# Optimization experiments

Measured on AMD Instinct MI355X. Metric: run time of the kernel, lower is better.

The kernel has to match this reference:

```python
import jax, jax.numpy as jnp
import numpy as np

N, E, F, EF, D, G = 25000, 100000, 32, 8, 64, 1000


def setup_inputs() -> dict:
    key = jax.random.key(0)
    ks = jax.random.split(key, 32)
    p = lambda k, shape: (jax.random.normal(k, shape, jnp.float32) * 0.05)
    inp = {
        "x": jax.random.normal(ks[0], (N, F), jnp.float32),
        "edge_index": jax.random.randint(ks[1], (2, E), 0, N, jnp.int64 if jax.config.jax_enable_x64 else jnp.int32),
        "edge_attr": jax.random.uniform(ks[2], (E, EF), jnp.float32),
        "batch": jnp.sort(jax.random.randint(ks[3], (N,), 0, G, jnp.int32)),
        # lin0
        "W0": p(ks[4], (F, D)), "b0": p(ks[5], (D,)),
        # edge MLP: Linear(EF, D) -> ReLU -> Linear(D, D*D)
        "We1": p(ks[6], (EF, D)), "be1": p(ks[7], (D,)),
        "We2": p(ks[8], (D, D * D)), "be2": p(ks[9], (D * D,)),
        # NNConv root weight + bias
        "Wroot": p(ks[10], (D, D)), "bconv": p(ks[11], (D,)),
        # GRU (single layer): gate order r, z, n
        "Wi": p(ks[12], (3 * D, D)), "Wh": p(ks[13], (3 * D, D)),
        "bi": p(ks[14], (3 * D,)), "bh": p(ks[15], (3 * D,)),
        # heads
        "W11": p(ks[16], (D, D)), "b11": p(ks[17], (D,)),
        "W12": p(ks[18], (D, D)), "b12": p(ks[19], (D,)),
        "W13": p(ks[20], (D, 1)), "b13": p(ks[21], (1,)),
        "W21": p(ks[22], (D, D)), "b21": p(ks[23], (D,)),
        "W22": p(ks[24], (D, D)), "b22": p(ks[25], (D,)),
        "W23": p(ks[26], (D, 1)), "b23": p(ks[27], (1,)),
    }
    return inp


def reference(x, edge_index, edge_attr, batch,
              W0, b0, We1, be1, We2, be2, Wroot, bconv,
              Wi, Wh, bi, bh,
              W11, b11, W12, b12, W13, b13,
              W21, b21, W22, b22, W23, b23):
    src, dst = edge_index[0], edge_index[1]
    # lin0 + relu
    x1 = jax.nn.relu(x @ W0 + b0)                      # [N, D]
    h = x1                                              # GRU hidden init
    # NNConv: dynamic per-edge weight via edge MLP
    ew = (jax.nn.relu(edge_attr @ We1 + be1) @ We2 + be2).reshape(E, D, D)
    msg = jnp.einsum('ei,eio->eo', x1[src], ew)        # per-edge matmul
    agg = jax.ops.segment_sum(msg, dst, num_segments=N)
    x2 = jax.nn.relu(x1 @ Wroot + agg + bconv)         # [N, D]
    # GRU single step (torch gate order: r, z, n)
    gi = x2 @ Wi.T + bi
    gh = h @ Wh.T + bh
    r = jax.nn.sigmoid(gi[:, :D] + gh[:, :D])
    z = jax.nn.sigmoid(gi[:, D:2 * D] + gh[:, D:2 * D])
    n = jnp.tanh(gi[:, 2 * D:] + r * gh[:, 2 * D:])
    hn = (1.0 - z) * n + z * h                          # [N, D]
    # graph pooling (scatter_add over batch)
    pooled = jax.ops.segment_sum(hn, batch, num_segments=G)  # [G, D]
    # two MLP heads
    x_1 = jax.nn.relu(pooled @ W11 + b11)
    x_1 = jax.nn.relu(x_1 @ W12 + b12)
    x_1 = x_1 @ W13 + b13
    x_2 = jax.nn.relu(pooled @ W21 + b21)
    x_2 = jax.nn.relu(x_2 @ W22 + b22)
    x_2 = x_2 @ W23 + b23
    return jnp.concatenate([x_1, x_2], axis=1)          # [G, 2]
```

## Files before the change

kernel.cpp:

```cpp
#include <hip/hip_runtime.h>
#include <hip/hip_bf16.h>
#include <hip/hip_fp16.h>

#define NN 25000
#define NE 100000
#define FIN 32
#define DD 64
#define NG 1000

typedef unsigned short u16;
typedef __attribute__((ext_vector_type(8))) short short8;
typedef __attribute__((ext_vector_type(8))) _Float16 f16x8;
typedef __attribute__((ext_vector_type(4))) float f32x4;

__device__ __forceinline__ u16 f2h(float f) {
    __half h = __float2half(f);
    return __builtin_bit_cast(u16, h);
}
__device__ __forceinline__ float h2f(u16 u) {
    __half h = __builtin_bit_cast(__half, u);
    return __half2float(h);
}
__device__ __forceinline__ f16x8 s2h(short8 v) { return __builtin_bit_cast(f16x8, v); }
__device__ __forceinline__ bool idx_is_i64(const int* e) {
    return (e[1] == 0) & (e[3] == 0) & (e[5] == 0) & (e[7] == 0) & (e[9] == 0);
}
__device__ __forceinline__ int ld_src(const int* e, int i, bool i64) {
    return i64 ? e[2 * i] : e[i];
}
__device__ __forceinline__ int ld_dst(const int* e, int i, bool i64) {
    return i64 ? e[2 * (NE + i)] : e[NE + i];
}

__global__ __launch_bounds__(256) void k_pre(const float* __restrict__ x,
                                             const float* __restrict__ W0,
                                             const float* __restrict__ b0,
                                             u16* __restrict__ x1b,
                                             const float* __restrict__ We2,
                                             const float* __restrict__ be2,
                                             float* __restrict__ agg,
                                             float* __restrict__ pooled,
                                             u16* __restrict__ Bt2,
                                             const float* __restrict__ Wi,
                                             const float* __restrict__ Wh,
                                             const float* __restrict__ Wroot,
                                             u16* __restrict__ Wib,
                                             u16* __restrict__ Whb,
                                             u16* __restrict__ Wrb,
                                             const float* __restrict__ W11,
                                             const float* __restrict__ W12,
                                             const float* __restrict__ W21,
                                             const float* __restrict__ W22,
                                             u16* __restrict__ W11b,
                                             u16* __restrict__ W12b,
                                             u16* __restrict__ W21b,
                                             u16* __restrict__ W22b) {
    __shared__ float sbuf[4096 + 512];
    int tid = threadIdx.x;
    if (blockIdx.x < 1563) {
        float* sW = sbuf;
        float* sx = sbuf + 4096;
        for (int i = tid; i < FIN * DD; i += 256) sW[i] = W0[i];
        int nbase = blockIdx.x * 16;
        for (int i = tid; i < 16 * FIN; i += 256) {
            int nl = i >> 5, f = i & 31;
            int n = nbase + nl;
            sx[i] = (n < NN) ? x[n * FIN + f] : 0.f;
        }
        __syncthreads();
        int lane = tid & 63, nl = tid >> 6;
        float bias = b0[lane];
        #pragma unroll
        for (int rr = 0; rr < 4; rr++) {
            int row = nl * 4 + rr;
            int n = nbase + row;
            if (n < NN) {
                float acc = bias;
                #pragma unroll
                for (int f = 0; f < FIN; f++) acc += sx[row * FIN + f] * sW[f * DD + lane];
                x1b[n * DD + lane] = f2h(fmaxf(acc, 0.f));
            }
        }
    } else if (blockIdx.x < 1628) {
        int kc = blockIdx.x - 1563;
        const float* src = (kc < 64) ? (We2 + kc * 4096) : be2;
        for (int i = tid; i < 4096; i += 256) sbuf[i] = src[i];
        __syncthreads();
        for (int m = tid; m < 4096; m += 256) {
            int f = m >> 9, ln = (m >> 3) & 63, j = m & 7;
            int s = f >> 2, c = f & 3;
            int o = c * 16 + (ln & 15);
            int rlow = s * 32 + (ln >> 4) * 8 + j;
            Bt2[kc * 4096 + m] = f2h(sbuf[rlow * 64 + o]);
        }
    } else {
        int tid0 = (blockIdx.x - 1628) * 256 + threadIdx.x;
        const int STR = 256 * 256;
        for (int i = tid0; i < NN * DD; i += STR) agg[i] = 0.f;
        for (int i = tid0; i < NG * DD; i += STR) pooled[i] = 0.f;
        for (int i = tid0; i < 12288; i += STR) {
            int fr = i >> 9, lane = (i >> 3) & 63, j = i & 7;
            int c = fr >> 1, kcx = fr & 1;
            int row = c * 16 + (lane & 15);
            int col = kcx * 32 + (lane >> 4) * 8 + j;
            Wib[i] = f2h(Wi[row * 64 + col]);
            Whb[i] = f2h(Wh[row * 64 + col]);
        }
        for (int i = tid0; i < 4096; i += STR) {
            int fr = i >> 9, lane = (i >> 3) & 63, j = i & 7;
            int c = fr >> 1, kcx = fr & 1;
            int row = c * 16 + (lane & 15);
            int col = kcx * 32 + (lane >> 4) * 8 + j;
            int idx = col * 64 + row;
            Wrb[i]  = f2h(Wroot[idx]);
            W11b[i] = f2h(W11[idx]);
            W12b[i] = f2h(W12[idx]);
            W21b[i] = f2h(W21[idx]);
            W22b[i] = f2h(W22[idx]);
        }
    }
}

__global__ __launch_bounds__(512, 4) void k_msg(const float* __restrict__ ea,
                                                const int* __restrict__ eidx,
                                                const float* __restrict__ We1,
                                                const float* __restrict__ be1,
                                                const u16* __restrict__ x1b,
                                                const u16* __restrict__ Bt2,
                                                float* __restrict__ agg) {
    __shared__ __align__(16) u16 sX[128 * 72];
    __shared__ __align__(16) u16 sTh[65 * 128 + 64];
    __shared__ float sWe1[8 * 64];
    __shared__ float sbe1[64];
    __shared__ int sDst[128];
    const int tid = threadIdx.x;
    const int lane = tid & 63, wv = tid >> 6;
    const int ll = lane & 15, quad = lane >> 4;
    const int rh = wv >> 2, cq = wv & 3;
    const int e0 = blockIdx.x * 128;
    const bool i64 = idx_is_i64(eidx);

    if (tid < 512) sWe1[tid] = We1[tid];
    if (tid < 64) sbe1[tid] = be1[tid];
    if (tid < 128) {
        sDst[tid] = (e0 + tid < NE) ? ld_dst(eidx, e0 + tid, i64) : 0;
        sTh[64 * 128 + tid] = 0x3C00;
    }

    const int el4 = tid >> 2, seg = tid & 3;
    const int eg4 = e0 + el4;
    {
        if (eg4 < NE) {
            int sv = ld_src(eidx, eg4, i64);
            const u16* xr = x1b + sv * 64 + seg * 16;
            *(uint4*)&sX[el4 * 72 + seg * 16]     = *(const uint4*)(xr);
            *(uint4*)&sX[el4 * 72 + seg * 16 + 8] = *(const uint4*)(xr + 8);
        } else {
            uint4 z = make_uint4(0, 0, 0, 0);
            *(uint4*)&sX[el4 * 72 + seg * 16]     = z;
            *(uint4*)&sX[el4 * 72 + seg * 16 + 8] = z;
        }
    }
    float eav[8];
    if (eg4 < NE) {
        f32x4 v0 = *(const f32x4*)(ea + eg4 * 8);
        f32x4 v1 = *(const f32x4*)(ea + eg4 * 8 + 4);
        #pragma unroll
        for (int f = 0; f < 4; f++) { eav[f] = v0[f]; eav[4 + f] = v1[f]; }
    } else {
        #pragma unroll
        for (int f = 0; f < 8; f++) eav[f] = 0.f;
    }
    __syncthreads();

    {
        int k0 = seg * 16;
        for (int kk = 0; kk < 16; kk++) {
            int k = k0 + kk;
            float acc = sbe1[k];
            #pragma unroll
            for (int f = 0; f < 8; f++) acc += eav[f] * sWe1[f * 64 + k];
            sTh[k * 128 + el4] = f2h((eg4 < NE) ? fmaxf(acc, 0.f) : 0.f);
        }
    }
    __syncthreads();

    short8 xa[4][2];
    #pragma unroll
    for (int rt = 0; rt < 4; rt++)
        #pragma unroll
        for (int s = 0; s < 2; s++)
            xa[rt][s] = *(const short8*)&sX[(rh * 64 + rt * 16 + ll) * 72 + s * 32 + quad * 8];

    f32x4 msg[4];
    #pragma unroll
    for (int rt = 0; rt < 4; rt++) msg[rt] = (f32x4){0.f, 0.f, 0.f, 0.f};

    const u16* gB0 = Bt2 + (0 * 4 + cq) * 512 + lane * 8;
    const u16* gB1 = Bt2 + (1 * 4 + cq) * 512 + lane * 8;
    const f32x4 zero = (f32x4){0.f, 0.f, 0.f, 0.f};
    const int tkoff = rh * 64 + quad * 4;

    #define LDR(dst, kcv, rtv) dst = *(const uint2*)&sTh[(kcv) * 128 + tkoff + (rtv) * 16];
    #define CVT(t, raw)                                                      \
        {                                                                    \
            __half2 _a = __builtin_bit_cast(__half2, (raw).x);               \
            __half2 _b = __builtin_bit_cast(__half2, (raw).y);               \
            float2 _fa = __half22float2(_a);                                 \
            float2 _fb = __half22float2(_b);                                 \
            t = (f32x4){_fa.x, _fa.y, _fb.x, _fb.y};                         \
        }

    short8 c00 = *(const short8*)(gB0);
    short8 c01 = *(const short8*)(gB1);
    short8 c10 = *(const short8*)(gB0 + 4096);
    short8 c11 = *(const short8*)(gB1 + 4096);
    uint2 tkA[4], tkB[4];
    #pragma unroll
    for (int rt = 0; rt < 4; rt++) LDR(tkA[rt], 0, rt);

    for (int kc = 0; kc < 62; kc += 2) {
        short8 n00 = *(const short8*)(gB0 + (kc + 2) * 4096);
        short8 n01 = *(const short8*)(gB1 + (kc + 2) * 4096);
        short8 n10 = *(const short8*)(gB0 + (kc + 3) * 4096);
        short8 n11 = *(const short8*)(gB1 + (kc + 3) * 4096);
        #pragma unroll
        for (int rt = 0; rt < 4; rt++) LDR(tkB[rt], kc + 1, rt);
        #pragma unroll
        for (int rt = 0; rt < 4; rt++) {
            f32x4 q0 = __builtin_amdgcn_mfma_f32_16x16x32_f16(s2h(xa[rt][0]), s2h(c00), zero, 0, 0, 0);
            f32x4 q1 = __builtin_amdgcn_mfma_f32_16x16x32_f16(s2h(xa[rt][1]), s2h(c01), zero, 0, 0, 0);
            f32x4 t; CVT(t, tkA[rt]);
            msg[rt] += t * q0;
            msg[rt] += t * q1;
        }
        #pragma unroll
        for (int rt = 0; rt < 4; rt++) LDR(tkA[rt], kc + 2, rt);
        #pragma unroll
        for (int rt = 0; rt < 4; rt++) {
            f32x4 q0 = __builtin_amdgcn_mfma_f32_16x16x32_f16(s2h(xa[rt][0]), s2h(c10), zero, 0, 0, 0);
            f32x4 q1 = __builtin_amdgcn_mfma_f32_16x16x32_f16(s2h(xa[rt][1]), s2h(c11), zero, 0, 0, 0);
            f32x4 t; CVT(t, tkB[rt]);
            msg[rt] += t * q0;
            msg[rt] += t * q1;
        }
        c00 = n00; c01 = n01; c10 = n10; c11 = n11;
    }
    {
        short8 n00 = *(const short8*)(gB0 + 64 * 4096);
        short8 n01 = *(const short8*)(gB1 + 64 * 4096);
        #pragma unroll
        for (int rt = 0; rt < 4; rt++) LDR(tkB[rt], 63, rt);
        #pragma unroll
        for (int rt = 0; rt < 4; rt++) {
            f32x4 q0 = __builtin_amdgcn_mfma_f32_16x16x32_f16(s2h(xa[rt][0]), s2h(c00), zero, 0, 0, 0);
            f32x4 q1 = __builtin_amdgcn_mfma_f32_16x16x32_f16(s2h(xa[rt][1]), s2h(c01), zero, 0, 0, 0);
            f32x4 t; CVT(t, tkA[rt]);
            msg[rt] += t * q0;
            msg[rt] += t * q1;
        }
        #pragma unroll
        for (int rt = 0; rt < 4; rt++) LDR(tkA[rt], 64, rt);
        #pragma unroll
        for (int rt = 0; rt < 4; rt++) {
            f32x4 q0 = __builtin_amdgcn_mfma_f32_16x16x32_f16(s2h(xa[rt][0]), s2h(c10), zero, 0, 0, 0);
            f32x4 q1 = __builtin_amdgcn_mfma_f32_16x16x32_f16(s2h(xa[rt][1]), s2h(c11), zero, 0, 0, 0);
            f32x4 t; CVT(t, tkB[rt]);
            msg[rt] += t * q0;
            msg[rt] += t * q1;
        }
        #pragma unroll
        for (int rt = 0; rt < 4; rt++) {
            f32x4 q0 = __builtin_amdgcn_mfma_f32_16x16x32_f16(s2h(xa[rt][0]), s2h(n00), zero, 0, 0, 0);
            f32x4 q1 = __builtin_amdgcn_mfma_f32_16x16x32_f16(s2h(xa[rt][1]), s2h(n01), zero, 0, 0, 0);
            f32x4 t; CVT(t, tkA[rt]);
            msg[rt] += t * q0;
            msg[rt] += t * q1;
        }
    }
    #undef LDR
    #undef CVT

    #pragma unroll
    for (int rt = 0; rt < 4; rt++) {
        #pragma unroll
        for (int r = 0; r < 4; r++) {
            int el = rh * 64 + rt * 16 + quad * 4 + r;
            int eg = e0 + el;
            if (eg < NE) {
                int d = sDst[el];
                atomicAdd(&agg[d * 64 + cq * 16 + ll], msg[rt][r]);
            }
        }
    }
}

__global__ __launch_bounds__(256) void k_gru(const u16* __restrict__ x1b,
                                             const float* __restrict__ agg,
                                             const u16* __restrict__ Wib,
                                             const u16* __restrict__ Whb,
                                             const u16* __restrict__ Wrb,
                                             const float* __restrict__ bconv,
                                             const float* __restrict__ bi,
                                             const float* __restrict__ bh,
                                             const int* __restrict__ batch,
                                             float* __restrict__ pooled) {
    __shared__ __align__(16) u16 sX2[64 * 72];
    __shared__ float hbuf[64 * 65];
    __shared__ int sBatch[64];
    const int tid = threadIdx.x;
    const int lane = tid & 63, wv = tid >> 6;
    const int ll = lane & 15, quad = lane >> 4;
    const int n0 = blockIdx.x * 64;

    if (tid < 64) {
        int n = n0 + tid;
        sBatch[tid] = (n < NN) ? batch[n] : -1;
    }

    short8 ha[2];
    {
        int n = n0 + wv * 16 + ll;
        #pragma unroll
        for (int kc = 0; kc < 2; kc++) {
            if (n < NN) ha[kc] = *(const short8*)(x1b + n * 64 + kc * 32 + quad * 8);
            else        ha[kc] = (short8){0,0,0,0,0,0,0,0};
        }
    }
    f32x4 acc1[4];
    #pragma unroll
    for (int c = 0; c < 4; c++) acc1[c] = (f32x4){0.f, 0.f, 0.f, 0.f};
    #pragma unroll
    for (int kc = 0; kc < 2; kc++) {
        #pragma unroll
        for (int c = 0; c < 4; c++) {
            short8 b = *(const short8*)&Wrb[(c * 2 + kc) * 512 + lane * 8];
            acc1[c] = __builtin_amdgcn_mfma_f32_16x16x32_f16(s2h(ha[kc]), s2h(b), acc1[c], 0, 0, 0);
        }
    }
    #pragma unroll
    for (int c = 0; c < 4; c++) {
        int col = c * 16 + ll;
        float bcv = bconv[col];
        #pragma unroll
        for (int r = 0; r < 4; r++) {
            int row = wv * 16 + quad * 4 + r;
            int n = n0 + row;
            float v = 0.f;
            if (n < NN) v = fmaxf(acc1[c][r] + agg[n * 64 + col] + bcv, 0.f);
            sX2[row * 72 + col] = f2h(v);
        }
    }
    __syncthreads();

    short8 xa[2];
    #pragma unroll
    for (int kc = 0; kc < 2; kc++)
        xa[kc] = *(const short8*)&sX2[(wv * 16 + ll) * 72 + kc * 32 + quad * 8];

    f32x4 agi[12], agh[12];
    #pragma unroll
    for (int c = 0; c < 12; c++) { agi[c] = (f32x4){0.f,0.f,0.f,0.f}; agh[c] = (f32x4){0.f,0.f,0.f,0.f}; }
    #pragma unroll
    for (int kc = 0; kc < 2; kc++) {
        #pragma unroll
        for (int c = 0; c < 12; c++) {
            short8 bi8 = *(const short8*)&Wib[(c * 2 + kc) * 512 + lane * 8];
            short8 bh8 = *(const short8*)&Whb[(c * 2 + kc) * 512 + lane * 8];
            agi[c] = __builtin_amdgcn_mfma_f32_16x16x32_f16(s2h(xa[kc]), s2h(bi8), agi[c], 0, 0, 0);
            agh[c] = __builtin_amdgcn_mfma_f32_16x16x32_f16(s2h(ha[kc]), s2h(bh8), agh[c], 0, 0, 0);
        }
    }

    float hnv[4][4];
    #pragma unroll
    for (int c0 = 0; c0 < 4; c0++) {
        int d = c0 * 16 + ll;
        float bir = bi[d],        bhr = bh[d];
        float biz = bi[64 + d],   bhz = bh[64 + d];
        float bin = bi[128 + d],  bhn = bh[128 + d];
        #pragma unroll
        for (int r = 0; r < 4; r++) {
            int row = wv * 16 + quad * 4 + r;
            int n = n0 + row;
            float gir = agi[c0][r] + bir,     ghr = agh[c0][r] + bhr;
            float giz = agi[c0 + 4][r] + biz, ghz = agh[c0 + 4][r] + bhz;
            float gin = agi[c0 + 8][r] + bin, ghn = agh[c0 + 8][r] + bhn;
            float rg = __fdividef(1.f, 1.f + __expf(-(gir + ghr)));
            float zg = __fdividef(1.f, 1.f + __expf(-(giz + ghz)));
            float xt = gin + rg * ghn;
            float e2 = __expf(2.f * xt);
            float ng = 1.f - __fdividef(2.f, e2 + 1.f);
            float hv = (n < NN) ? h2f(x1b[n * 64 + d]) : 0.f;
            hnv[c0][r] = (n < NN) ? ((1.f - zg) * ng + zg * hv) : 0.f;
        }
    }
    __syncthreads();

    #pragma unroll
    for (int c0 = 0; c0 < 4; c0++) {
        int d = c0 * 16 + ll;
        #pragma unroll
        for (int r = 0; r < 4; r++) {
            int row = wv * 16 + quad * 4 + r;
            hbuf[row * 65 + d] = hnv[c0][r];
        }
    }
    __syncthreads();

    {
        int d = lane;
        float sum = 0.f;
        int pb = sBatch[wv * 16];
        #pragma unroll
        for (int rr = 0; rr < 16; rr++) {
            int row = wv * 16 + rr;
            int b = sBatch[row];
            float v = hbuf[row * 65 + d];
            if (b != pb) {
                if (pb >= 0) atomicAdd(&pooled[pb * 64 + d], sum);
                sum = v; pb = b;
            } else {
                sum += v;
            }
        }
        if (pb >= 0) atomicAdd(&pooled[pb * 64 + d], sum);
    }
}

__global__ __launch_bounds__(256) void k_heads(const float* __restrict__ pooled,
                                               const u16* __restrict__ W11b, const float* __restrict__ b11,
                                               const u16* __restrict__ W12b, const float* __restrict__ b12,
                                               const float* __restrict__ W13, const float* __restrict__ b13,
                                               const u16* __restrict__ W21b, const float* __restrict__ b21,
                                               const u16* __restrict__ W22b, const float* __restrict__ b22,
                                               const float* __restrict__ W23, const float* __restrict__ b23,
                                               float* __restrict__ out) {
    __shared__ __align__(16) u16 sY[64 * 72];
    const int tid = threadIdx.x;
    const int lane = tid & 63, wv = tid >> 6;
    const int ll = lane & 15, quad = lane >> 4;
    const int g0 = blockIdx.x * 64;
    const f32x4 zero = (f32x4){0.f, 0.f, 0.f, 0.f};

    short8 pa[2];
    {
        int g = g0 + wv * 16 + ll;
        #pragma unroll
        for (int kc = 0; kc < 2; kc++) {
            if (g < NG) {
                const float* pr = pooled + g * 64 + kc * 32 + quad * 8;
                f32x4 v0 = *(const f32x4*)(pr);
                f32x4 v1 = *(const f32x4*)(pr + 4);
                short8 s;
                #pragma unroll
                for (int j = 0; j < 4; j++) {
                    s[j]     = (short)f2h(v0[j]);
                    s[4 + j] = (short)f2h(v1[j]);
                }
                pa[kc] = s;
            } else {
                pa[kc] = (short8){0,0,0,0,0,0,0,0};
            }
        }
    }

    const u16* W1s[2] = {W11b, W21b}; const float* b1s[2] = {b11, b21};
    const u16* W2s[2] = {W12b, W22b}; const float* b2s[2] = {b12, b22};
    const float* W3s[2] = {W13, W23}; const float* b3s[2] = {b13, b23};

    #pragma unroll
    for (int hd = 0; hd < 2; hd++) {
        f32x4 a1[4];
        #pragma unroll
        for (int c = 0; c < 4; c++) a1[c] = zero;
        #pragma unroll
        for (int kc = 0; kc < 2; kc++)
            #pragma unroll
            for (int c = 0; c < 4; c++) {
                short8 b = *(const short8*)&W1s[hd][(c * 2 + kc) * 512 + lane * 8];
                a1[c] = __builtin_amdgcn_mfma_f32_16x16x32_f16(s2h(pa[kc]), s2h(b), a1[c], 0, 0, 0);
            }
        #pragma unroll
        for (int c = 0; c < 4; c++) {
            int col = c * 16 + ll;
            float bv = b1s[hd][col];
            #pragma unroll
            for (int r = 0; r < 4; r++) {
                int row = wv * 16 + quad * 4 + r;
                sY[row * 72 + col] = f2h(fmaxf(a1[c][r] + bv, 0.f));
            }
        }
        __syncthreads();
        short8 ya[2];
        #pragma unroll
        for (int kc = 0; kc < 2; kc++)
            ya[kc] = *(const short8*)&sY[(wv * 16 + ll) * 72 + kc * 32 + quad * 8];
        f32x4 a2[4];
        #pragma unroll
        for (int c = 0; c < 4; c++) a2[c] = zero;
        #pragma unroll
        for (int kc = 0; kc < 2; kc++)
            #pragma unroll
            for (int c = 0; c < 4; c++) {
                short8 b = *(const short8*)&W2s[hd][(c * 2 + kc) * 512 + lane * 8];
                a2[c] = __builtin_amdgcn_mfma_f32_16x16x32_f16(s2h(ya[kc]), s2h(b), a2[c], 0, 0, 0);
            }
        #pragma unroll
        for (int r = 0; r < 4; r++) {
            float part = 0.f;
            #pragma unroll
            for (int c = 0; c < 4; c++) {
                int col = c * 16 + ll;
                part += fmaxf(a2[c][r] + b2s[hd][col], 0.f) * W3s[hd][col];
            }
            part += __shfl_xor(part, 1, 64);
            part += __shfl_xor(part, 2, 64);
            part += __shfl_xor(part, 4, 64);
            part += __shfl_xor(part, 8, 64);
            if (ll == 0) {
                int g = g0 + wv * 16 + quad * 4 + r;
                if (g < NG) out[g * 2 + hd] = part + b3s[hd][0];
            }
        }
        __syncthreads();
    }
}

extern "C" void kernel_launch(void* const* d_in, const int* in_sizes, int n_in,
                              void* d_out, int out_size, void* d_ws, size_t ws_size,
                              hipStream_t stream) {
    const float* x     = (const float*)d_in[0];
    const int* eidx    = (const int*)d_in[1];
    const float* ea    = (const float*)d_in[2];
    const int* batch   = (const int*)d_in[3];
    const float* W0    = (const float*)d_in[4];  const float* b0    = (const float*)d_in[5];
    const float* We1   = (const float*)d_in[6];  const float* be1   = (const float*)d_in[7];
    const float* We2   = (const float*)d_in[8];  const float* be2   = (const float*)d_in[9];
    const float* Wroot = (const float*)d_in[10]; const float* bconv = (const float*)d_in[11];
    const float* Wi    = (const float*)d_in[12]; const float* Wh    = (const float*)d_in[13];
    const float* bi    = (const float*)d_in[14]; const float* bh    = (const float*)d_in[15];
    const float* W11   = (const float*)d_in[16]; const float* b11   = (const float*)d_in[17];
    const float* W12   = (const float*)d_in[18]; const float* b12   = (const float*)d_in[19];
    const float* W13   = (const float*)d_in[20]; const float* b13   = (const float*)d_in[21];
    const float* W21   = (const float*)d_in[22]; const float* b21   = (const float*)d_in[23];
    const float* W22   = (const float*)d_in[24]; const float* b22   = (const float*)d_in[25];
    const float* W23   = (const float*)d_in[26]; const float* b23   = (const float*)d_in[27];
    float* out = (float*)d_out;

    char* ws = (char*)d_ws;
    float* agg    = (float*)(ws);
    u16*   x1b    = (u16*)(ws + 6400000);
    u16*   Bt2    = (u16*)(ws + 9600000);
    float* pooled = (float*)(ws + 10132480);
    u16*   Wib    = (u16*)(ws + 10388480);
    u16*   Whb    = (u16*)(ws + 10413056);
    u16*   Wrb    = (u16*)(ws + 10437632);
    u16*   W11b   = (u16*)(ws + 10445824);
    u16*   W12b   = (u16*)(ws + 10454016);
    u16*   W21b   = (u16*)(ws + 10462208);
    u16*   W22b   = (u16*)(ws + 10470400);

    hipLaunchKernelGGL(k_pre, dim3(1884), dim3(256), 0, stream,
                       x, W0, b0, x1b, We2, be2, agg, pooled, Bt2,
                       Wi, Wh, Wroot, Wib, Whb, Wrb,
                       W11, W12, W21, W22, W11b, W12b, W21b, W22b);
    hipLaunchKernelGGL(k_msg, dim3(782), dim3(512), 0, stream, ea, eidx, We1, be1, x1b, Bt2, agg);
    hipLaunchKernelGGL(k_gru, dim3(391), dim3(256), 0, stream, x1b, agg,
                       Wib, Whb, Wrb, bconv, bi, bh, batch, pooled);
    hipLaunchKernelGGL(k_heads, dim3(16), dim3(256), 0, stream, pooled,
                       W11b, b11, W12b, b12, W13, b13, W21b, b21, W22b, b22, W23, b23, out);
}
```

Before: 224.1 us.

## Fuse four kernels into one cooperative persistent kernel with grid syncs

Replaces the four separate launches (preprocessing, edge messages, GRU, heads) with a single cooperative kernel that loops over virtual blocks and separates the stages with grid-wide syncs. The goal is to remove inter-kernel launch gaps and tail drain between stages. The grid size is capped by the occupancy query (at most 512 blocks of 512 threads). The trade-offs are grid.sync overhead, lower parallelism in some stages such as the 391-tile GRU stage that uses only half the threads, and reduced occupancy from the launch bounds. The old four-kernel path stays as a fallback if the cooperative launch fails.

```diff
diff --git a/kernel.cpp b/kernel.cpp
--- a/kernel.cpp
+++ b/kernel.cpp
@@ -1,6 +1,9 @@
 #include <hip/hip_runtime.h>
 #include <hip/hip_bf16.h>
 #include <hip/hip_fp16.h>
+#include <hip/hip_cooperative_groups.h>
+
+namespace cg = cooperative_groups;
 
 #define NN 25000
 #define NE 100000
@@ -30,6 +33,489 @@
 }
 __device__ __forceinline__ int ld_dst(const int* e, int i, bool i64) {
     return i64 ? e[2 * (NE + i)] : e[NE + i];
+}
+
+__global__ __launch_bounds__(512, 4) void k_mega(
+    const float* __restrict__ x, const int* __restrict__ eidx,
+    const float* __restrict__ ea, const int* __restrict__ batch,
+    const float* __restrict__ W0, const float* __restrict__ b0,
+    const float* __restrict__ We1, const float* __restrict__ be1,
+    const float* __restrict__ We2, const float* __restrict__ be2,
+    const float* __restrict__ Wroot, const float* __restrict__ bconv,
+    const float* __restrict__ Wi, const float* __restrict__ Wh,
+    const float* __restrict__ bi, const float* __restrict__ bh,
+    const float* __restrict__ W13, const float* __restrict__ b13,
+    const float* __restrict__ W23, const float* __restrict__ b23,
+    const float* __restrict__ b11, const float* __restrict__ b12,
+    const float* __restrict__ b21, const float* __restrict__ b22,
+    const float* __restrict__ W11, const float* __restrict__ W12,
+    const float* __restrict__ W21, const float* __restrict__ W22,
+    float* __restrict__ out,
+    float* __restrict__ agg, u16* __restrict__ x1b, u16* __restrict__ Bt2,
+    float* __restrict__ pooled,
+    u16* __restrict__ Wib, u16* __restrict__ Whb, u16* __restrict__ Wrb,
+    u16* __restrict__ W11b, u16* __restrict__ W12b,
+    u16* __restrict__ W21b, u16* __restrict__ W22b) {
+    cg::grid_group grid = cg::this_grid();
+    __shared__ __align__(16) char smem[38400];
+    const int tid = threadIdx.x;
+    const int bid = blockIdx.x;
+    const int G = gridDim.x;
+    const int lane = tid & 63, ll = lane & 15, quad = lane >> 4;
+    const f32x4 zero = (f32x4){0.f, 0.f, 0.f, 0.f};
+
+    {
+        float* sbuf = (float*)smem;
+        for (int vb = bid; vb < 1628; vb += G) {
+            __syncthreads();
+            if (vb < 1563) {
+                float* sW = sbuf;
+                float* sx = sbuf + 2048;
+                for (int i = tid; i < FIN * DD; i += 512) sW[i] = W0[i];
+                int nbase = vb * 16;
+                for (int i = tid; i < 16 * FIN; i += 512) {
+                    int nl = i >> 5, f = i & 31;
+                    int n = nbase + nl;
+                    sx[i] = (n < NN) ? x[n * FIN + f] : 0.f;
+                }
+                __syncthreads();
+                int nl8 = tid >> 6;
+                float bias = b0[lane];
+                #pragma unroll
+                for (int rr = 0; rr < 2; rr++) {
+                    int row = nl8 * 2 + rr;
+                    int n = nbase + row;
+                    if (n < NN) {
+                        float acc = bias;
+                        #pragma unroll
+                        for (int f = 0; f < FIN; f++) acc += sx[row * FIN + f] * sW[f * DD + lane];
+                        x1b[n * DD + lane] = f2h(fmaxf(acc, 0.f));
+                    }
+                }
+            } else {
+                int kc = vb - 1563;
+                const float* src = (kc < 64) ? (We2 + kc * 4096) : be2;
+                for (int i = tid; i < 4096; i += 512) sbuf[i] = src[i];
+                __syncthreads();
+                for (int m = tid; m < 4096; m += 512) {
+                    int f = m >> 9, ln = (m >> 3) & 63, j = m & 7;
+                    int s = f >> 2, c = f & 3;
+                    int o = c * 16 + (ln & 15);
+                    int rlow = s * 32 + (ln >> 4) * 8 + j;
+                    Bt2[kc * 4096 + m] = f2h(sbuf[rlow * 64 + o]);
+                }
+            }
+        }
+        int gt = bid * 512 + tid;
+        int STR = G * 512;
+        for (int i = gt; i < NN * DD; i += STR) agg[i] = 0.f;
+        for (int i = gt; i < NG * DD; i += STR) pooled[i] = 0.f;
+        for (int i = gt; i < 12288; i += STR) {
+            int fr = i >> 9, ln = (i >> 3) & 63, j = i & 7;
+            int c = fr >> 1, kcx = fr & 1;
+            int row = c * 16 + (ln & 15);
+            int col = kcx * 32 + (ln >> 4) * 8 + j;
+            Wib[i] = f2h(Wi[row * 64 + col]);
+            Whb[i] = f2h(Wh[row * 64 + col]);
+        }
+        for (int i = gt; i < 4096; i += STR) {
+            int fr = i >> 9, ln = (i >> 3) & 63, j = i & 7;
+            int c = fr >> 1, kcx = fr & 1;
+            int row = c * 16 + (ln & 15);
+            int col = kcx * 32 + (ln >> 4) * 8 + j;
+            int idx = col * 64 + row;
+            Wrb[i]  = f2h(Wroot[idx]);
+            W11b[i] = f2h(W11[idx]);
+            W12b[i] = f2h(W12[idx]);
+            W21b[i] = f2h(W21[idx]);
+            W22b[i] = f2h(W22[idx]);
+        }
+    }
+    grid.sync();
+
+    {
+        u16* sX    = (u16*)smem;
+        u16* sTh   = (u16*)(smem + 18432);
+        float* sWe1 = (float*)(smem + 35200);
+        float* sbe1 = (float*)(smem + 37248);
+        int* sDst  = (int*)(smem + 37504);
+        const int wv = tid >> 6;
+        const int rh = wv >> 2, cq = wv & 3;
+        const bool i64 = idx_is_i64(eidx);
+
+        for (int vt = bid; vt < 782; vt += G) {
+            __syncthreads();
+            const int e0 = vt * 128;
+            sWe1[tid] = We1[tid];
+            if (tid < 64) sbe1[tid] = be1[tid];
+            if (tid < 128) {
+                sDst[tid] = (e0 + tid < NE) ? ld_dst(eidx, e0 + tid, i64) : 0;
+                sTh[64 * 128 + tid] = 0x3C00;
+            }
+            const int el4 = tid >> 2, seg = tid & 3;
+            const int eg4 = e0 + el4;
+            {
+                if (eg4 < NE) {
+                    int sv = ld_src(eidx, eg4, i64);
+                    const u16* xr = x1b + sv * 64 + seg * 16;
+                    *(uint4*)&sX[el4 * 72 + seg * 16]     = *(const uint4*)(xr);
+                    *(uint4*)&sX[el4 * 72 + seg * 16 + 8] = *(const uint4*)(xr + 8);
+                } else {
+                    uint4 z = make_uint4(0, 0, 0, 0);
+                    *(uint4*)&sX[el4 * 72 + seg * 16]     = z;
+                    *(uint4*)&sX[el4 * 72 + seg * 16 + 8] = z;
+                }
+            }
+            float eav[8];
+            if (eg4 < NE) {
+                f32x4 v0 = *(const f32x4*)(ea + eg4 * 8);
+                f32x4 v1 = *(const f32x4*)(ea + eg4 * 8 + 4);
+                #pragma unroll
+                for (int f = 0; f < 4; f++) { eav[f] = v0[f]; eav[4 + f] = v1[f]; }
+            } else {
+                #pragma unroll
+                for (int f = 0; f < 8; f++) eav[f] = 0.f;
+            }
+            __syncthreads();
+            {
+                int k0 = seg * 16;
+                for (int kk = 0; kk < 16; kk++) {
+                    int k = k0 + kk;
+                    float acc = sbe1[k];
+                    #pragma unroll
+                    for (int f = 0; f < 8; f++) acc += eav[f] * sWe1[f * 64 + k];
+                    sTh[k * 128 + el4] = f2h((eg4 < NE) ? fmaxf(acc, 0.f) : 0.f);
+                }
+            }
+            __syncthreads();
+
+            short8 xa[4][2];
+            #pragma unroll
+            for (int rt = 0; rt < 4; rt++)
+                #pragma unroll
+                for (int s = 0; s < 2; s++)
+                    xa[rt][s] = *(const short8*)&sX[(rh * 64 + rt * 16 + ll) * 72 + s * 32 + quad * 8];
+
+            f32x4 msg[4];
+            #pragma unroll
+            for (int rt = 0; rt < 4; rt++) msg[rt] = zero;
+
+            const u16* gB0 = Bt2 + (0 * 4 + cq) * 512 + lane * 8;
+            const u16* gB1 = Bt2 + (1 * 4 + cq) * 512 + lane * 8;
+            const int tkoff = rh * 64 + quad * 4;
+
+            #define LDR(dst, kcv, rtv) dst = *(const uint2*)&sTh[(kcv) * 128 + tkoff + (rtv) * 16];
+            #define CVT(t, raw)                                                      \
+                {                                                                    \
+                    __half2 _a = __builtin_bit_cast(__half2, (raw).x);               \
+                    __half2 _b = __builtin_bit_cast(__half2, (raw).y);               \
+                    float2 _fa = __half22float2(_a);                                 \
+                    float2 _fb = __half22float2(_b);                                 \
+                    t = (f32x4){_fa.x, _fa.y, _fb.x, _fb.y};                         \
+                }
+
+            short8 c00 = *(const short8*)(gB0);
+            short8 c01 = *(const short8*)(gB1);
+            short8 c10 = *(const short8*)(gB0 + 4096);
+            short8 c11 = *(const short8*)(gB1 + 4096);
+            uint2 tkA[4], tkB[4];
+            #pragma unroll
+            for (int rt = 0; rt < 4; rt++) LDR(tkA[rt], 0, rt);
+
+            for (int kc = 0; kc < 62; kc += 2) {
+                short8 n00 = *(const short8*)(gB0 + (kc + 2) * 4096);
+                short8 n01 = *(const short8*)(gB1 + (kc + 2) * 4096);
+                short8 n10 = *(const short8*)(gB0 + (kc + 3) * 4096);
+                short8 n11 = *(const short8*)(gB1 + (kc + 3) * 4096);
+                #pragma unroll
+                for (int rt = 0; rt < 4; rt++) LDR(tkB[rt], kc + 1, rt);
+                #pragma unroll
+                for (int rt = 0; rt < 4; rt++) {
+                    f32x4 q0 = __builtin_amdgcn_mfma_f32_16x16x32_f16(s2h(xa[rt][0]), s2h(c00), zero, 0, 0, 0);
+                    f32x4 q1 = __builtin_amdgcn_mfma_f32_16x16x32_f16(s2h(xa[rt][1]), s2h(c01), zero, 0, 0, 0);
+                    f32x4 t; CVT(t, tkA[rt]);
+                    msg[rt] += t * q0;
+                    msg[rt] += t * q1;
+                }
+                #pragma unroll
+                for (int rt = 0; rt < 4; rt++) LDR(tkA[rt], kc + 2, rt);
+                #pragma unroll
+                for (int rt = 0; rt < 4; rt++) {
+                    f32x4 q0 = __builtin_amdgcn_mfma_f32_16x16x32_f16(s2h(xa[rt][0]), s2h(c10), zero, 0, 0, 0);
+                    f32x4 q1 = __builtin_amdgcn_mfma_f32_16x16x32_f16(s2h(xa[rt][1]), s2h(c11), zero, 0, 0, 0);
+                    f32x4 t; CVT(t, tkB[rt]);
+                    msg[rt] += t * q0;
+                    msg[rt] += t * q1;
+                }
+                c00 = n00; c01 = n01; c10 = n10; c11 = n11;
+            }
+            {
+                short8 n00 = *(const short8*)(gB0 + 64 * 4096);
+                short8 n01 = *(const short8*)(gB1 + 64 * 4096);
+                #pragma unroll
+                for (int rt = 0; rt < 4; rt++) LDR(tkB[rt], 63, rt);
+                #pragma unroll
+                for (int rt = 0; rt < 4; rt++) {
+                    f32x4 q0 = __builtin_amdgcn_mfma_f32_16x16x32_f16(s2h(xa[rt][0]), s2h(c00), zero, 0, 0, 0);
+                    f32x4 q1 = __builtin_amdgcn_mfma_f32_16x16x32_f16(s2h(xa[rt][1]), s2h(c01), zero, 0, 0, 0);
+                    f32x4 t; CVT(t, tkA[rt]);
+                    msg[rt] += t * q0;
+                    msg[rt] += t * q1;
+                }
+                #pragma unroll
+                for (int rt = 0; rt < 4; rt++) LDR(tkA[rt], 64, rt);
+                #pragma unroll
+                for (int rt = 0; rt < 4; rt++) {
+                    f32x4 q0 = __builtin_amdgcn_mfma_f32_16x16x32_f16(s2h(xa[rt][0]), s2h(c10), zero, 0, 0, 0);
+                    f32x4 q1 = __builtin_amdgcn_mfma_f32_16x16x32_f16(s2h(xa[rt][1]), s2h(c11), zero, 0, 0, 0);
+                    f32x4 t; CVT(t, tkB[rt]);
+                    msg[rt] += t * q0;
+                    msg[rt] += t * q1;
+                }
+                #pragma unroll
+                for (int rt = 0; rt < 4; rt++) {
+                    f32x4 q0 = __builtin_amdgcn_mfma_f32_16x16x32_f16(s2h(xa[rt][0]), s2h(n00), zero, 0, 0, 0);
+                    f32x4 q1 = __builtin_amdgcn_mfma_f32_16x16x32_f16(s2h(xa[rt][1]), s2h(n01), zero, 0, 0, 0);
+                    f32x4 t; CVT(t, tkA[rt]);
+                    msg[rt] += t * q0;
+                    msg[rt] += t * q1;
+                }
+            }
+            #undef LDR
+            #undef CVT
+
+            #pragma unroll
+            for (int rt = 0; rt < 4; rt++) {
+                #pragma unroll
+                for (int r = 0; r < 4; r++) {
+                    int el = rh * 64 + rt * 16 + quad * 4 + r;
+                    int eg = e0 + el;
+                    if (eg < NE) {
+                        int d = sDst[el];
+                        atomicAdd(&agg[d * 64 + cq * 16 + ll], msg[rt][r]);
+                    }
+                }
+            }
+        }
+    }
+    grid.sync();
+
+    {
+        u16* sX2 = (u16*)smem;
+        float* hb = (float*)(smem + 9216);
+        int* sBatch = (int*)(smem + 25856);
+        for (int vt = bid; vt < 391; vt += G) {
+            __syncthreads();
+            const bool act = tid < 256;
+            const int n0 = vt * 64;
+            const int wv = (tid >> 6) & 3;
+            short8 ha[2];
+            float hnv[4][4];
+            if (act) {
+                if (tid < 64) {
+                    int n = n0 + tid;
+                    sBatch[tid] = (n < NN) ? batch[n] : -1;
+                }
+                int n = n0 + wv * 16 + ll;
+                #pragma unroll
+                for (int kc = 0; kc < 2; kc++) {
+                    if (n < NN) ha[kc] = *(const short8*)(x1b + n * 64 + kc * 32 + quad * 8);
+                    else        ha[kc] = (short8){0,0,0,0,0,0,0,0};
+                }
+                f32x4 acc1[4];
+                #pragma unroll
+                for (int c = 0; c < 4; c++) acc1[c] = zero;
+                #pragma unroll
+                for (int kc = 0; kc < 2; kc++) {
+                    #pragma unroll
+                    for (int c = 0; c < 4; c++) {
+                        short8 b = *(const short8*)&Wrb[(c * 2 + kc) * 512 + lane * 8];
+                        acc1[c] = __builtin_amdgcn_mfma_f32_16x16x32_f16(s2h(ha[kc]), s2h(b), acc1[c], 0, 0, 0);
+                    }
+                }
+                #pragma unroll
+                for (int c = 0; c < 4; c++) {
+                    int col = c * 16 + ll;
+                    float bcv = bconv[col];
+                    #pragma unroll
+                    for (int r = 0; r < 4; r++) {
+                        int row = wv * 16 + quad * 4 + r;
+                        int n2 = n0 + row;
+                        float v = 0.f;
+                        if (n2 < NN) v = fmaxf(acc1[c][r] + agg[n2 * 64 + col] + bcv, 0.f);
+                        sX2[row * 72 + col] = f2h(v);
+                    }
+                }
+            }
+            __syncthreads();
+            if (act) {
+                short8 xg[2];
+                #pragma unroll
+                for (int kc = 0; kc < 2; kc++)
+                    xg[kc] = *(const short8*)&sX2[(wv * 16 + ll) * 72 + kc * 32 + quad * 8];
+                f32x4 agi[12], agh[12];
+                #pragma unroll
+                for (int c = 0; c < 12; c++) { agi[c] = zero; agh[c] = zero; }
+                #pragma unroll
+                for (int kc = 0; kc < 2; kc++) {
+                    #pragma unroll
+                    for (int c = 0; c < 12; c++) {
+                        short8 bi8 = *(const short8*)&Wib[(c * 2 + kc) * 512 + lane * 8];
+                        short8 bh8 = *(const short8*)&Whb[(c * 2 + kc) * 512 + lane * 8];
+                        agi[c] = __builtin_amdgcn_mfma_f32_16x16x32_f16(s2h(xg[kc]), s2h(bi8), agi[c], 0, 0, 0);
+                        agh[c] = __builtin_amdgcn_mfma_f32_16x16x32_f16(s2h(ha[kc]), s2h(bh8), agh[c], 0, 0, 0);
+                    }
+                }
+                #pragma unroll
+                for (int c0 = 0; c0 < 4; c0++) {
+                    int d = c0 * 16 + ll;
+                    float bir = bi[d],        bhr = bh[d];
+                    float biz = bi[64 + d],   bhz = bh[64 + d];
+                    float bin = bi[128 + d],  bhn = bh[128 + d];
+                    #pragma unroll
+                    for (int r = 0; r < 4; r++) {
+                        int row = wv * 16 + quad * 4 + r;
+                        int n2 = n0 + row;
+                        float gir = agi[c0][r] + bir,     ghr = agh[c0][r] + bhr;
+                        float giz = agi[c0 + 4][r] + biz, ghz = agh[c0 + 4][r] + bhz;
+                        float gin = agi[c0 + 8][r] + bin, ghn = agh[c0 + 8][r] + bhn;
+                        float rg = __fdividef(1.f, 1.f + __expf(-(gir + ghr)));
+                        float zg = __fdividef(1.f, 1.f + __expf(-(giz + ghz)));
+                        float xt = gin + rg * ghn;
+                        float e2 = __expf(2.f * xt);
+                        float ng = 1.f - __fdividef(2.f, e2 + 1.f);
+                        float hv = (n2 < NN) ? h2f(x1b[n2 * 64 + d]) : 0.f;
+                        hnv[c0][r] = (n2 < NN) ? ((1.f - zg) * ng + zg * hv) : 0.f;
+                    }
+                }
+            }
+            __syncthreads();
+            if (act) {
+                #pragma unroll
+                for (int c0 = 0; c0 < 4; c0++) {
+                    int d = c0 * 16 + ll;
+                    #pragma unroll
+                    for (int r = 0; r < 4; r++) {
+                        int row = wv * 16 + quad * 4 + r;
+                        hb[row * 65 + d] = hnv[c0][r];
+                    }
+                }
+            }
+            __syncthreads();
+            if (act) {
+                int d = lane;
+                float sum = 0.f;
+                int pb = sBatch[wv * 16];
+                #pragma unroll
+                for (int rr = 0; rr < 16; rr++) {
+                    int row = wv * 16 + rr;
+                    int b = sBatch[row];
+                    float v = hb[row * 65 + d];
+                    if (b != pb) {
+                        if (pb >= 0) atomicAdd(&pooled[pb * 64 + d], sum);
+                        sum = v; pb = b;
+                    } else {
+                        sum += v;
+                    }
+                }
+                if (pb >= 0) atomicAdd(&pooled[pb * 64 + d], sum);
+            }
+        }
+    }
+    grid.sync();
+
+    {
+        u16* sY = (u16*)smem;
+        const u16* W1s[2] = {W11b, W21b}; const float* b1s[2] = {b11, b21};
+        const u16* W2s[2] = {W12b, W22b}; const float* b2s[2] = {b12, b22};
+        const float* W3s[2] = {W13, W23}; const float* b3s[2] = {b13, b23};
+        for (int vt = bid; vt < 16; vt += G) {
+            __syncthreads();
+            const bool act = tid < 256;
+            const int wv = (tid >> 6) & 3;
+            const int g0 = vt * 64;
+            short8 pa[2];
+            if (act) {
+                int g = g0 + wv * 16 + ll;
+                #pragma unroll
+                for (int kc = 0; kc < 2; kc++) {
+                    if (g < NG) {
+                        const float* pr = pooled + g * 64 + kc * 32 + quad * 8;
+                        f32x4 v0 = *(const f32x4*)(pr);
+                        f32x4 v1 = *(const f32x4*)(pr + 4);
+                        short8 s;
+                        #pragma unroll
+                        for (int j = 0; j < 4; j++) {
+                            s[j]     = (short)f2h(v0[j]);
+                            s[4 + j] = (short)f2h(v1[j]);
+                        }
+                        pa[kc] = s;
+                    } else {
+                        pa[kc] = (short8){0,0,0,0,0,0,0,0};
+                    }
+                }
+            }
+            for (int hd = 0; hd < 2; hd++) {
+                if (act) {
+                    f32x4 a1[4];
+                    #pragma unroll
+                    for (int c = 0; c < 4; c++) a1[c] = zero;
+                    #pragma unroll
+                    for (int kc = 0; kc < 2; kc++)
+                        #pragma unroll
+                        for (int c = 0; c < 4; c++) {
+                            short8 b = *(const short8*)&W1s[hd][(c * 2 + kc) * 512 + lane * 8];
+                            a1[c] = __builtin_amdgcn_mfma_f32_16x16x32_f16(s2h(pa[kc]), s2h(b), a1[c], 0, 0, 0);
+                        }
+                    #pragma unroll
+                    for (int c = 0; c < 4; c++) {
+                        int col = c * 16 + ll;
+                        float bv = b1s[hd][col];
+                        #pragma unroll
+                        for (int r = 0; r < 4; r++) {
+                            int row = wv * 16 + quad * 4 + r;
+                            sY[row * 72 + col] = f2h(fmaxf(a1[c][r] + bv, 0.f));
+                        }
+                    }
+                }
+                __syncthreads();
+                if (act) {
+                    short8 ya[2];
+                    #pragma unroll
+                    for (int kc = 0; kc < 2; kc++)
+                        ya[kc] = *(const short8*)&sY[(wv * 16 + ll) * 72 + kc * 32 + quad * 8];
+                    f32x4 a2[4];
+                    #pragma unroll
+                    for (int c = 0; c < 4; c++) a2[c] = zero;
+                    #pragma unroll
+                    for (int kc = 0; kc < 2; kc++)
+                        #pragma unroll
+                        for (int c = 0; c < 4; c++) {
+                            short8 b = *(const short8*)&W2s[hd][(c * 2 + kc) * 512 + lane * 8];
+                            a2[c] = __builtin_amdgcn_mfma_f32_16x16x32_f16(s2h(ya[kc]), s2h(b), a2[c], 0, 0, 0);
+                        }
+                    #pragma unroll
+                    for (int r = 0; r < 4; r++) {
+                        float part = 0.f;
+                        #pragma unroll
+                        for (int c = 0; c < 4; c++) {
+                            int col = c * 16 + ll;
+                            part += fmaxf(a2[c][r] + b2s[hd][col], 0.f) * W3s[hd][col];
+                        }
+                        part += __shfl_xor(part, 1, 64);
+                        part += __shfl_xor(part, 2, 64);
+                        part += __shfl_xor(part, 4, 64);
+                        part += __shfl_xor(part, 8, 64);
+                        if (ll == 0) {
+                            int g = g0 + wv * 16 + quad * 4 + r;
+                            if (g < NG) out[g * 2 + hd] = part + b3s[hd][0];
+                        }
+                    }
+                }
+                __syncthreads();
+            }
+        }
+    }
 }
 
 __global__ __launch_bounds__(256) void k_pre(const float* __restrict__ x,
@@ -146,7 +632,6 @@
         sDst[tid] = (e0 + tid < NE) ? ld_dst(eidx, e0 + tid, i64) : 0;
         sTh[64 * 128 + tid] = 0x3C00;
     }
-
     const int el4 = tid >> 2, seg = tid & 3;
     const int eg4 = e0 + el4;
     {
@@ -172,7 +657,6 @@
         for (int f = 0; f < 8; f++) eav[f] = 0.f;
     }
     __syncthreads();
-
     {
         int k0 = seg * 16;
         for (int kk = 0; kk < 16; kk++) {
@@ -317,7 +801,6 @@
         int n = n0 + tid;
         sBatch[tid] = (n < NN) ? batch[n] : -1;
     }
-
     short8 ha[2];
     {
         int n = n0 + wv * 16 + ll;
@@ -464,11 +947,9 @@
             }
         }
     }
-
     const u16* W1s[2] = {W11b, W21b}; const float* b1s[2] = {b11, b21};
     const u16* W2s[2] = {W12b, W22b}; const float* b2s[2] = {b12, b22};
     const float* W3s[2] = {W13, W23}; const float* b3s[2] = {b13, b23};
-
     #pragma unroll
     for (int hd = 0; hd < 2; hd++) {
         f32x4 a1[4];
@@ -561,13 +1042,37 @@
     u16*   W21b   = (u16*)(ws + 10462208);
     u16*   W22b   = (u16*)(ws + 10470400);
 
-    hipLaunchKernelGGL(k_pre, dim3(1884), dim3(256), 0, stream,
-                       x, W0, b0, x1b, We2, be2, agg, pooled, Bt2,
-                       Wi, Wh, Wroot, Wib, Whb, Wrb,
-                       W11, W12, W21, W22, W11b, W12b, W21b, W22b);
-    hipLaunchKernelGGL(k_msg, dim3(782), dim3(512), 0, stream, ea, eidx, We1, be1, x1b, Bt2, agg);
-    hipLaunchKernelGGL(k_gru, dim3(391), dim3(256), 0, stream, x1b, agg,
-                       Wib, Whb, Wrb, bconv, bi, bh, batch, pooled);
-    hipLaunchKernelGGL(k_heads, dim3(16), dim3(256), 0, stream, pooled,
-                       W11b, b11, W12b, b12, W13, b13, W21b, b21, W22b, b22, W23, b23, out);
+    int maxB = 0;
+    int G = 512;
+    if (hipOccupancyMaxActiveBlocksPerMultiprocessor(&maxB, k_mega, 512, 0) == hipSuccess && maxB >= 1) {
+        long cap = (long)maxB * 256;
+        G = (cap < 512) ? (int)cap : 512;
+    }
+    void* kargs[] = {
+        (void*)&x, (void*)&eidx, (void*)&ea, (void*)&batch,
+        (void*)&W0, (void*)&b0, (void*)&We1, (void*)&be1, (void*)&We2, (void*)&be2,
+        (void*)&Wroot, (void*)&bconv, (void*)&Wi, (void*)&Wh, (void*)&bi, (void*)&bh,
+        (void*)&W13, (void*)&b13, (void*)&W23, (void*)&b23,
+        (void*)&b11, (void*)&b12, (void*)&b21, (void*)&b22,
+        (void*)&W11, (void*)&W12, (void*)&W21, (void*)&W22,
+        (void*)&out,
+        (void*)&agg, (void*)&x1b, (void*)&Bt2, (void*)&pooled,
+        (void*)&Wib, (void*)&Whb, (void*)&Wrb,
+        (void*)&W11b, (void*)&W12b, (void*)&W21b, (void*)&W22b
+    };
+    hipError_t err = hipLaunchCooperativeKernel((void*)k_mega, dim3(G), dim3(512),
+                                                kargs, 0, stream);
+    if (err != hipSuccess) {
+        (void)hipGetLastError();
+        hipLaunchKernelGGL(k_pre, dim3(1884), dim3(256), 0, stream,
+                           x, W0, b0, x1b, We2, be2, agg, pooled, Bt2,
+                           Wi, Wh, Wroot, Wib, Whb, Wrb,
+                           W11, W12, W21, W22, W11b, W12b, W21b, W22b);
+        hipLaunchKernelGGL(k_msg, dim3(782), dim3(512), 0, stream,
+                           ea, eidx, We1, be1, x1b, Bt2, agg);
+        hipLaunchKernelGGL(k_gru, dim3(391), dim3(256), 0, stream, x1b, agg,
+                           Wib, Whb, Wrb, bconv, bi, bh, batch, pooled);
+        hipLaunchKernelGGL(k_heads, dim3(16), dim3(256), 0, stream, pooled,
+                           W11b, b11, W12b, b12, W13, b13, W21b, b21, W22b, b22, W23, b23, out);
+    }
 }
```

Result: slower. 466.8 us (+108.3%).
